# Optimization experiments

Hardware: AMD Instinct MI355X
Metric: run time of the kernel (lower is better)

## Reference

```python
import jax, jax.numpy as jnp
import numpy as np

B, N, D, H = 4, 2048, 256, 8
DH = D // H  # 32
EPS = 1e-5


def layernorm(x, g, b):
    mu = jnp.mean(x, axis=-1, keepdims=True)
    var = jnp.mean(jnp.square(x - mu), axis=-1, keepdims=True)
    return (x - mu) * jax.lax.rsqrt(var + EPS) * g + b


def setup_inputs() -> dict:
    key = jax.random.key(0)
    ks = jax.random.split(key, 16)
    s = 1.0 / np.sqrt(D)
    p = lambda k: jax.random.uniform(k, (D, D), jnp.float32, -s, s)
    return {
        "qdt": jax.random.normal(ks[0], (B, N, D), jnp.float32),
        "boxes": jax.random.normal(ks[1], (B, N, D), jnp.float32),
        "mask": jax.random.randint(ks[2], (N, N), 0, 2, jnp.int32),
        "Wq": p(ks[3]), "bq": jnp.zeros((D,), jnp.float32),
        "Wk": p(ks[4]), "bk": jnp.zeros((D,), jnp.float32),
        "Wv": p(ks[5]), "bv": jnp.zeros((D,), jnp.float32),
        "Wo": p(ks[6]), "bo": jnp.zeros((D,), jnp.float32),
        "W1": p(ks[7]), "b1": jnp.zeros((D,), jnp.float32),
        "W2": p(ks[8]), "b2": jnp.zeros((D,), jnp.float32),
        "g1": jnp.ones((D,), jnp.float32), "be1": jnp.zeros((D,), jnp.float32),
        "g2": jnp.ones((D,), jnp.float32), "be2": jnp.zeros((D,), jnp.float32),
    }


def reference(qdt, boxes, mask, Wq, bq, Wk, bk, Wv, bv, Wo, bo,
              W1, b1, W2, b2, g1, be1, g2, be2):
    # q = k = tgt = boxes + qdt  (dropout in eval mode -> identity)
    x = boxes + qdt  # [B,N,D]
    q = (x @ Wq + bq).reshape(B, N, H, DH)
    k = (x @ Wk + bk).reshape(B, N, H, DH)
    v = (x @ Wv + bv).reshape(B, N, H, DH)
    scores = jnp.einsum('bqhd,bkhd->bhqk', q, k) / np.sqrt(DH)
    # masked_fill(mask==0, -inf) then sigmoid  ==  sigmoid gated to 0 where masked
    attn = jnp.where(mask.astype(bool)[None, None, :, :],
                     jax.nn.sigmoid(scores), 0.0)
    o = jnp.einsum('bhqk,bkhd->bqhd', attn, v).reshape(B, N, D)
    attn_out = o @ Wo + bo
    tgt = layernorm(x + attn_out, g1, be1)
    ff = jax.nn.relu(tgt @ W1 + b1) @ W2 + b2
    tgt = layernorm(tgt + ff, g2, be2)
    return tgt
```

## Files before the change

### kernel.cpp

```cpp
#include <hip/hip_runtime.h>
#include <hip/hip_bf16.h>

typedef unsigned short u16;
typedef unsigned int u32;
typedef __attribute__((ext_vector_type(8))) short bf16x8;
typedef __attribute__((ext_vector_type(4))) float f32x4;

#define BB 4
#define NN 2048
#define DD 256
#define HH 8
#define LAMBDA (-0.2550351f)

__device__ inline u16 bfu(float f) {
  __hip_bfloat16 h = __float2bfloat16(f);
  return *reinterpret_cast<u16*>(&h);
}
__device__ inline bf16x8 asfrag(uint4 v) { return __builtin_bit_cast(bf16x8, v); }

__global__ __launch_bounds__(256) void prep_kernel(
    const float* __restrict__ qdt, const float* __restrict__ boxes,
    const int* __restrict__ mask,
    const float* __restrict__ Wq, const float* __restrict__ Wk, const float* __restrict__ Wv,
    const float* __restrict__ Wo, const float* __restrict__ W1, const float* __restrict__ W2,
    const float* __restrict__ bq, const float* __restrict__ bk, const float* __restrict__ bv,
    float* __restrict__ xp, u16* __restrict__ xb, unsigned char* __restrict__ m8,
    u16* __restrict__ wqkvT, u16* __restrict__ woT, u16* __restrict__ w1T, u16* __restrict__ w2T,
    float* __restrict__ bqkv) {
  const int bid = blockIdx.x, t = threadIdx.x;
  if (bid < 2048) {
    int i = bid * 256 + t;
    int row = i >> 6, q = i & 63;
    float4 a = ((const float4*)qdt)[i];
    float4 b = ((const float4*)boxes)[i];
    float4 v = make_float4(a.x + b.x, a.y + b.y, a.z + b.z, a.w + b.w);
    ((ushort4*)xb)[i] = make_ushort4(bfu(v.x), bfu(v.y), bfu(v.z), bfu(v.w));
    float* xr = xp + (size_t)row * 256;
    xr[((4*q+0) & 15) * 16 + ((4*q+0) >> 4)] = v.x;
    xr[((4*q+1) & 15) * 16 + ((4*q+1) >> 4)] = v.y;
    xr[((4*q+2) & 15) * 16 + ((4*q+2) >> 4)] = v.z;
    xr[((4*q+3) & 15) * 16 + ((4*q+3) >> 4)] = v.w;
  } else if (bid < 6144) {
    int i = (bid - 2048) * 256 + t;
    int4 m = ((const int4*)mask)[i];
    ((uchar4*)m8)[i] = make_uchar4((unsigned char)m.x, (unsigned char)m.y,
                                   (unsigned char)m.z, (unsigned char)m.w);
  } else {
    int i = (bid - 6144) * 256 + t;
    if (i < 196608) {
      int n = i >> 8, k = i & 255;
      const float* src = (n < 256) ? Wq : (n < 512 ? Wk : Wv);
      wqkvT[i] = bfu(src[k * 256 + (n & 255)]);
    } else if (i < 262144) {
      int j = i - 196608; int n = j >> 8, k = j & 255;
      woT[j] = bfu(Wo[k * 256 + n]);
    } else if (i < 327680) {
      int j = i - 262144; int n = j >> 8, k = j & 255;
      w1T[j] = bfu(W1[k * 256 + n]);
    } else if (i < 393216) {
      int j = i - 327680; int n = j >> 8, k = j & 255;
      w2T[j] = bfu(W2[k * 256 + n]);
    } else if (i < 393984) {
      int n = i - 393216;
      bqkv[n] = (n < 256) ? bq[n] : (n < 512 ? bk[n - 256] : bv[n - 512]);
    }
  }
}

__global__ __launch_bounds__(256) void gemm_qkvt_kernel(
    const u16* __restrict__ xb, const u16* __restrict__ wqkvT,
    const float* __restrict__ bqkv,
    u16* __restrict__ qout, u16* __restrict__ kout, u16* __restrict__ vtout) {
  __shared__ u16 At[64][264];
  __shared__ u16 Bs[64][264];
  const int bid = blockIdx.x;
  const bool isqk = bid < 1024;
  const u16* A  = isqk ? xb : (wqkvT + 512 * 256);
  const u16* Bt = isqk ? wqkvT : xb;
  const int m0 = isqk ? (bid >> 3) * 64 : ((bid - 1024) >> 7) * 64;
  const int n0 = isqk ? (bid & 7) * 64 : ((bid - 1024) & 127) * 64;
  const int t = threadIdx.x;
  {
    const int row = t >> 2, cb = (t & 3) * 64;
    const u16* ga = A  + (size_t)(m0 + row) * 256 + cb;
    const u16* gb = Bt + (size_t)(n0 + row) * 256 + cb;
#pragma unroll
    for (int i = 0; i < 8; ++i) {
      *(int4*)&At[row][cb + i * 8] = *(const int4*)(ga + i * 8);
      *(int4*)&Bs[row][cb + i * 8] = *(const int4*)(gb + i * 8);
    }
  }
  __syncthreads();
  const int w = t >> 6, l = t & 63, g = l >> 4, c = l & 15;
  f32x4 acc[4] = {};
#pragma unroll
  for (int kk = 0; kk < 256; kk += 32) {
    bf16x8 af = *(const bf16x8*)&At[w * 16 + c][kk + g * 8];
#pragma unroll
    for (int j = 0; j < 4; ++j) {
      bf16x8 bfr = *(const bf16x8*)&Bs[j * 16 + c][kk + g * 8];
      acc[j] = __builtin_amdgcn_mfma_f32_16x16x32_bf16(af, bfr, acc[j], 0, 0, 0);
    }
  }
  if (isqk) {
    if (n0 < 256) {
#pragma unroll
      for (int j = 0; j < 4; ++j)
#pragma unroll
        for (int r = 0; r < 4; ++r) {
          int m = m0 + w * 16 + g * 4 + r, n = n0 + j * 16 + c;
          qout[(size_t)m * 256 + n] = bfu((acc[j][r] + bqkv[n]) * LAMBDA);
        }
    } else {
#pragma unroll
      for (int j = 0; j < 4; ++j)
#pragma unroll
        for (int r = 0; r < 4; ++r) {
          int m = m0 + w * 16 + g * 4 + r, n = n0 + j * 16 + c;
          int ch = n - 256;
          kout[(size_t)((m >> 11) * 8 + (ch >> 5)) * 65536 + (size_t)(m & 2047) * 32 + (ch & 31)]
              = bfu(acc[j][r] + bqkv[n]);
        }
    }
  } else {
#pragma unroll
    for (int j = 0; j < 4; ++j)
#pragma unroll
      for (int r = 0; r < 4; ++r) {
        int m = m0 + w * 16 + g * 4 + r;
        int n = n0 + j * 16 + c;
        vtout[(size_t)m * 8192 + n] = bfu(acc[j][r] + bqkv[512 + m]);
      }
  }
}

__global__ __launch_bounds__(256) void attn_kernel(
    const u16* __restrict__ qb,
    const u16* __restrict__ kb,
    const u16* __restrict__ vtb,
    const unsigned char* __restrict__ m8,
    u16* __restrict__ ob) {
  __shared__ u32 Klds[2][64][20];
  __shared__ u32 Vlds[2][32][36];
  __shared__ unsigned char Mlds[2][128][64];
  __shared__ u32 Plds[4][32][36];

  const int bid = blockIdx.x;
  const int qt = bid & 15, h = (bid >> 4) & 7, b = bid >> 7;
  const int q0 = qt * 128;
  const int t = threadIdx.x, w = t >> 6, l = t & 63, g = l >> 4, c = l & 15;

  const bf16x8 qf0 = asfrag(*(const uint4*)(qb + (size_t)(b * NN + q0 + 32 * w + c) * 256 + h * 32 + 8 * g));
  const bf16x8 qf1 = asfrag(*(const uint4*)(qb + (size_t)(b * NN + q0 + 32 * w + 16 + c) * 256 + h * 32 + 8 * g));
  f32x4 oacc[2][2] = {};

  const int srowK = t >> 2, ssegK = t & 3;
  const int srowV = t >> 3, ssegV = t & 7;
  const int msrow = t >> 1, mhalf = t & 1;
  const u16* kg = kb + (size_t)(b * 8 + h) * 65536 + srowK * 32 + ssegK * 8;
  const u16* vg = vtb + (size_t)(h * 32 + srowV) * 8192 + (size_t)b * NN + ssegV * 8;
  const unsigned char* mg = m8 + (size_t)(q0 + msrow) * NN + mhalf * 32;

  const int rotM = 8 * (msrow & 7);
  const int mbA0 = (32 * mhalf + rotM) & 63, mbA1 = (mbA0 + 8) & 63;
  const int mbB0 = (mbA0 + 16) & 63,         mbB1 = (mbA0 + 24) & 63;

  uint4 krg = *(const uint4*)kg;
  uint4 vrg = *(const uint4*)vg;
  uint4 mrgA = *(const uint4*)mg;
  uint4 mrgB = *(const uint4*)(mg + 16);
  *(uint4*)&Klds[0][srowK][ssegK * 4] = krg;
  *(uint4*)&Vlds[0][srowV][ssegV * 4] = vrg;
  *(uint2*)&Mlds[0][msrow][mbA0] = make_uint2(mrgA.x, mrgA.y);
  *(uint2*)&Mlds[0][msrow][mbA1] = make_uint2(mrgA.z, mrgA.w);
  *(uint2*)&Mlds[0][msrow][mbB0] = make_uint2(mrgB.x, mrgB.y);
  *(uint2*)&Mlds[0][msrow][mbB1] = make_uint2(mrgB.z, mrgB.w);
  __syncthreads();

  const f32x4 zf = {0.f, 0.f, 0.f, 0.f};
  u32* Pw = &Plds[w][0][0];

  for (int it = 0; it < 32; ++it) {
    const int cur = it & 1;
    if (it < 31) {
      const int kt = (it + 1) * 64;
      krg = *(const uint4*)(kg + (size_t)kt * 32);
      vrg = *(const uint4*)(vg + kt);
      mrgA = *(const uint4*)(mg + kt);
      mrgB = *(const uint4*)(mg + kt + 16);
    }
#pragma unroll
    for (int tt = 0; tt < 4; ++tt) {
      bf16x8 kf = asfrag(*(const uint4*)&Klds[cur][16 * tt + c][4 * g]);
      f32x4 s0 = __builtin_amdgcn_mfma_f32_16x16x32_bf16(kf, qf0, zf, 0, 0, 0);
      f32x4 s1 = __builtin_amdgcn_mfma_f32_16x16x32_bf16(kf, qf1, zf, 0, 0, 0);
      const int mpos = (16 * tt + 4 * g + 8 * (c & 7)) & 63;
      u32 mdw0 = *(const u32*)&Mlds[cur][32 * w + c][mpos];
      u32 mdw1 = *(const u32*)&Mlds[cur][32 * w + 16 + c][mpos];
      {
        float p0 = (float)(mdw0 & 0xffu) * __builtin_amdgcn_rcpf(1.f + __builtin_amdgcn_exp2f(s0[0]));
        float p1 = (float)((mdw0 >> 8) & 0xffu) * __builtin_amdgcn_rcpf(1.f + __builtin_amdgcn_exp2f(s0[1]));
        float p2 = (float)((mdw0 >> 16) & 0xffu) * __builtin_amdgcn_rcpf(1.f + __builtin_amdgcn_exp2f(s0[2]));
        float p3 = (float)(mdw0 >> 24) * __builtin_amdgcn_rcpf(1.f + __builtin_amdgcn_exp2f(s0[3]));
        u32 w0, w1;
        asm("v_cvt_pk_bf16_f32 %0, %1, %2" : "=v"(w0) : "v"(p0), "v"(p1));
        asm("v_cvt_pk_bf16_f32 %0, %1, %2" : "=v"(w1) : "v"(p2), "v"(p3));
        *(uint2*)&Pw[c * 36 + 8 * tt + 2 * g] = make_uint2(w0, w1);
      }
      {
        float p0 = (float)(mdw1 & 0xffu) * __builtin_amdgcn_rcpf(1.f + __builtin_amdgcn_exp2f(s1[0]));
        float p1 = (float)((mdw1 >> 8) & 0xffu) * __builtin_amdgcn_rcpf(1.f + __builtin_amdgcn_exp2f(s1[1]));
        float p2 = (float)((mdw1 >> 16) & 0xffu) * __builtin_amdgcn_rcpf(1.f + __builtin_amdgcn_exp2f(s1[2]));
        float p3 = (float)(mdw1 >> 24) * __builtin_amdgcn_rcpf(1.f + __builtin_amdgcn_exp2f(s1[3]));
        u32 w0, w1;
        asm("v_cvt_pk_bf16_f32 %0, %1, %2" : "=v"(w0) : "v"(p0), "v"(p1));
        asm("v_cvt_pk_bf16_f32 %0, %1, %2" : "=v"(w1) : "v"(p2), "v"(p3));
        *(uint2*)&Pw[(16 + c) * 36 + 8 * tt + 2 * g] = make_uint2(w0, w1);
      }
    }
    asm volatile("s_waitcnt lgkmcnt(0)" ::: "memory");
    __builtin_amdgcn_sched_barrier(0);
#pragma unroll
    for (int kk = 0; kk < 2; ++kk) {
      bf16x8 pf0 = asfrag(*(const uint4*)&Pw[c * 36 + 16 * kk + 4 * g]);
      bf16x8 pf1 = asfrag(*(const uint4*)&Pw[(16 + c) * 36 + 16 * kk + 4 * g]);
#pragma unroll
      for (int d0 = 0; d0 < 2; ++d0) {
        bf16x8 vf = asfrag(*(const uint4*)&Vlds[cur][16 * d0 + c][16 * kk + 4 * g]);
        oacc[0][d0] = __builtin_amdgcn_mfma_f32_16x16x32_bf16(pf0, vf, oacc[0][d0], 0, 0, 0);
        oacc[1][d0] = __builtin_amdgcn_mfma_f32_16x16x32_bf16(pf1, vf, oacc[1][d0], 0, 0, 0);
      }
    }
    if (it < 31) {
      *(uint4*)&Klds[cur ^ 1][srowK][ssegK * 4] = krg;
      *(uint4*)&Vlds[cur ^ 1][srowV][ssegV * 4] = vrg;
      *(uint2*)&Mlds[cur ^ 1][msrow][mbA0] = make_uint2(mrgA.x, mrgA.y);
      *(uint2*)&Mlds[cur ^ 1][msrow][mbA1] = make_uint2(mrgA.z, mrgA.w);
      *(uint2*)&Mlds[cur ^ 1][msrow][mbB0] = make_uint2(mrgB.x, mrgB.y);
      *(uint2*)&Mlds[cur ^ 1][msrow][mbB1] = make_uint2(mrgB.z, mrgB.w);
    }
    __syncthreads();
  }

#pragma unroll
  for (int f = 0; f < 2; ++f) {
    const size_t obase = (size_t)(b * NN + q0 + 32 * w + 16 * f) * 256 + h * 32;
#pragma unroll
    for (int d0 = 0; d0 < 2; ++d0)
#pragma unroll
      for (int r = 0; r < 4; ++r)
        ob[obase + (size_t)(4 * g + r) * 256 + 16 * d0 + c] = bfu(oacc[f][d0][r]);
  }
}

__global__ __launch_bounds__(256) void tail_kernel(
    const u16* __restrict__ obuf, const u16* __restrict__ woT,
    const u16* __restrict__ w1T, const u16* __restrict__ w2T,
    const float* __restrict__ xp,
    const float* __restrict__ bo, const float* __restrict__ b1, const float* __restrict__ b2,
    const float* __restrict__ g1, const float* __restrict__ be1,
    const float* __restrict__ g2, const float* __restrict__ be2,
    float* __restrict__ out) {
  __shared__ u16 A[32][264];
  __shared__ float PS1[32][4], PS2[32][4];
  const int t = threadIdx.x, w = t >> 6, l = t & 63, g = l >> 4, c = l & 15;
  const int m0 = blockIdx.x * 32;
  const int n0 = w * 64;
  const f32x4 zf4 = {0.f, 0.f, 0.f, 0.f};

  {
    const int srow = t >> 3, sseg = t & 7;
#pragma unroll
    for (int i = 0; i < 4; ++i) {
      uint4 v = *(const uint4*)(obuf + (size_t)(m0 + srow) * 256 + (sseg + 8 * i) * 8);
      *(uint4*)&A[srow][(sseg + 8 * i) * 8] = v;
    }
  }
  __syncthreads();

  f32x4 acc[2][4], t1[2][4];
  float mean[2][4], inv[2][4];

#pragma unroll
  for (int rg = 0; rg < 2; ++rg)
#pragma unroll
    for (int j = 0; j < 4; ++j) acc[rg][j] = zf4;
#pragma unroll
  for (int kk = 0; kk < 256; kk += 32) {
    bf16x8 af0 = *(const bf16x8*)&A[c][kk + 8 * g];
    bf16x8 af1 = *(const bf16x8*)&A[16 + c][kk + 8 * g];
#pragma unroll
    for (int j = 0; j < 4; ++j) {
      bf16x8 bfr = asfrag(*(const uint4*)(woT + (size_t)(n0 + 16 * j + c) * 256 + kk + 8 * g));
      acc[0][j] = __builtin_amdgcn_mfma_f32_16x16x32_bf16(af0, bfr, acc[0][j], 0, 0, 0);
      acc[1][j] = __builtin_amdgcn_mfma_f32_16x16x32_bf16(af1, bfr, acc[1][j], 0, 0, 0);
    }
  }
  {
    float bov[4];
#pragma unroll
    for (int j = 0; j < 4; ++j) bov[j] = bo[n0 + 16 * j + c];
#pragma unroll
    for (int rg = 0; rg < 2; ++rg)
#pragma unroll
      for (int r = 0; r < 4; ++r) {
        const int rl = 16 * rg + 4 * g + r;
        float4 xq = ((const float4*)(xp + (size_t)(m0 + rl) * 256 + c * 16))[w];
        float xa[4] = {xq.x, xq.y, xq.z, xq.w};
        float a1 = 0.f, a2 = 0.f;
#pragma unroll
        for (int j = 0; j < 4; ++j) {
          float z = acc[rg][j][r] + bov[j] + xa[j];
          t1[rg][j][r] = z;
          a1 += z; a2 += z * z;
        }
#pragma unroll
        for (int off = 1; off < 16; off <<= 1) {
          a1 += __shfl_xor(a1, off);
          a2 += __shfl_xor(a2, off);
        }
        if (c == 0) { PS1[rl][w] = a1; PS2[rl][w] = a2; }
      }
  }
  __syncthreads();
#pragma unroll
  for (int rg = 0; rg < 2; ++rg)
#pragma unroll
    for (int r = 0; r < 4; ++r) {
      const int rl = 16 * rg + 4 * g + r;
      float s1 = PS1[rl][0] + PS1[rl][1] + PS1[rl][2] + PS1[rl][3];
      float s2 = PS2[rl][0] + PS2[rl][1] + PS2[rl][2] + PS2[rl][3];
      mean[rg][r] = s1 * (1.f / 256.f);
      inv[rg][r] = rsqrtf(s2 * (1.f / 256.f) - mean[rg][r] * mean[rg][r] + 1e-5f);
    }
#pragma unroll
  for (int j = 0; j < 4; ++j) {
    const int n = n0 + 16 * j + c;
    const float gv = g1[n], bev = be1[n];
#pragma unroll
    for (int rg = 0; rg < 2; ++rg)
#pragma unroll
      for (int r = 0; r < 4; ++r) {
        float v = (t1[rg][j][r] - mean[rg][r]) * inv[rg][r] * gv + bev;
        t1[rg][j][r] = v;
        A[16 * rg + 4 * g + r][n] = bfu(v);
      }
  }
  __syncthreads();

#pragma unroll
  for (int rg = 0; rg < 2; ++rg)
#pragma unroll
    for (int j = 0; j < 4; ++j) acc[rg][j] = zf4;
#pragma unroll
  for (int kk = 0; kk < 256; kk += 32) {
    bf16x8 af0 = *(const bf16x8*)&A[c][kk + 8 * g];
    bf16x8 af1 = *(const bf16x8*)&A[16 + c][kk + 8 * g];
#pragma unroll
    for (int j = 0; j < 4; ++j) {
      bf16x8 bfr = asfrag(*(const uint4*)(w1T + (size_t)(n0 + 16 * j + c) * 256 + kk + 8 * g));
      acc[0][j] = __builtin_amdgcn_mfma_f32_16x16x32_bf16(af0, bfr, acc[0][j], 0, 0, 0);
      acc[1][j] = __builtin_amdgcn_mfma_f32_16x16x32_bf16(af1, bfr, acc[1][j], 0, 0, 0);
    }
  }
  __syncthreads();
#pragma unroll
  for (int j = 0; j < 4; ++j) {
    const int n = n0 + 16 * j + c;
    const float bv = b1[n];
#pragma unroll
    for (int rg = 0; rg < 2; ++rg)
#pragma unroll
      for (int r = 0; r < 4; ++r) {
        float v = acc[rg][j][r] + bv;
        A[16 * rg + 4 * g + r][n] = bfu(v > 0.f ? v : 0.f);
      }
  }
  __syncthreads();

#pragma unroll
  for (int rg = 0; rg < 2; ++rg)
#pragma unroll
    for (int j = 0; j < 4; ++j) acc[rg][j] = zf4;
#pragma unroll
  for (int kk = 0; kk < 256; kk += 32) {
    bf16x8 af0 = *(const bf16x8*)&A[c][kk + 8 * g];
    bf16x8 af1 = *(const bf16x8*)&A[16 + c][kk + 8 * g];
#pragma unroll
    for (int j = 0; j < 4; ++j) {
      bf16x8 bfr = asfrag(*(const uint4*)(w2T + (size_t)(n0 + 16 * j + c) * 256 + kk + 8 * g));
      acc[0][j] = __builtin_amdgcn_mfma_f32_16x16x32_bf16(af0, bfr, acc[0][j], 0, 0, 0);
      acc[1][j] = __builtin_amdgcn_mfma_f32_16x16x32_bf16(af1, bfr, acc[1][j], 0, 0, 0);
    }
  }
  {
    float b2v[4];
#pragma unroll
    for (int j = 0; j < 4; ++j) b2v[j] = b2[n0 + 16 * j + c];
#pragma unroll
    for (int rg = 0; rg < 2; ++rg)
#pragma unroll
      for (int r = 0; r < 4; ++r) {
        const int rl = 16 * rg + 4 * g + r;
        float a1 = 0.f, a2 = 0.f;
#pragma unroll
        for (int j = 0; j < 4; ++j) {
          float z = acc[rg][j][r] + b2v[j] + t1[rg][j][r];
          t1[rg][j][r] = z;
          a1 += z; a2 += z * z;
        }
#pragma unroll
        for (int off = 1; off < 16; off <<= 1) {
          a1 += __shfl_xor(a1, off);
          a2 += __shfl_xor(a2, off);
        }
        if (c == 0) { PS1[rl][w] = a1; PS2[rl][w] = a2; }
      }
  }
  __syncthreads();
#pragma unroll
  for (int rg = 0; rg < 2; ++rg)
#pragma unroll
    for (int r = 0; r < 4; ++r) {
      const int rl = 16 * rg + 4 * g + r;
      float s1 = PS1[rl][0] + PS1[rl][1] + PS1[rl][2] + PS1[rl][3];
      float s2 = PS2[rl][0] + PS2[rl][1] + PS2[rl][2] + PS2[rl][3];
      mean[rg][r] = s1 * (1.f / 256.f);
      inv[rg][r] = rsqrtf(s2 * (1.f / 256.f) - mean[rg][r] * mean[rg][r] + 1e-5f);
    }
#pragma unroll
  for (int j = 0; j < 4; ++j) {
    const int n = n0 + 16 * j + c;
    const float gv = g2[n], bev = be2[n];
#pragma unroll
    for (int rg = 0; rg < 2; ++rg)
#pragma unroll
      for (int r = 0; r < 4; ++r)
        out[(size_t)(m0 + 16 * rg + 4 * g + r) * 256 + n]
            = (t1[rg][j][r] - mean[rg][r]) * inv[rg][r] * gv + bev;
  }
}

extern "C" void kernel_launch(void* const* d_in, const int* in_sizes, int n_in,
                              void* d_out, int out_size, void* d_ws, size_t ws_size,
                              hipStream_t stream) {
  const float* qdt   = (const float*)d_in[0];
  const float* boxes = (const float*)d_in[1];
  const int*   mask  = (const int*)d_in[2];
  const float* Wq = (const float*)d_in[3];
  const float* bq = (const float*)d_in[4];
  const float* Wk = (const float*)d_in[5];
  const float* bk = (const float*)d_in[6];
  const float* Wv = (const float*)d_in[7];
  const float* bv = (const float*)d_in[8];
  const float* Wo = (const float*)d_in[9];
  const float* bo = (const float*)d_in[10];
  const float* W1 = (const float*)d_in[11];
  const float* b1 = (const float*)d_in[12];
  const float* W2 = (const float*)d_in[13];
  const float* b2 = (const float*)d_in[14];
  const float* g1  = (const float*)d_in[15];
  const float* be1 = (const float*)d_in[16];
  const float* g2  = (const float*)d_in[17];
  const float* be2 = (const float*)d_in[18];

  char* ws = (char*)d_ws;
  float* xp    = (float*)(ws + 0);
  u16*   xb    = (u16*)  (ws + 8388608);
  u16*   qbuf  = (u16*)  (ws + 12582912);
  u16*   kbuf  = (u16*)  (ws + 16777216);
  u16*   vtbuf = (u16*)  (ws + 20971520);
  u16*   obuf  = (u16*)  (ws + 25165824);
  u16*   wqkvT = (u16*)  (ws + 46137344);
  u16*   woT   = (u16*)  (ws + 46530560);
  u16*   w1T   = (u16*)  (ws + 46661632);
  u16*   w2T   = (u16*)  (ws + 46792704);
  float* bqkv  = (float*)(ws + 46923776);
  unsigned char* m8 = (unsigned char*)(ws + 46926848);

  prep_kernel<<<7683, 256, 0, stream>>>(qdt, boxes, mask, Wq, Wk, Wv, Wo, W1, W2,
                                        bq, bk, bv, xp, xb, m8,
                                        wqkvT, woT, w1T, w2T, bqkv);
  gemm_qkvt_kernel<<<1536, 256, 0, stream>>>(xb, wqkvT, bqkv, qbuf, kbuf, vtbuf);
  attn_kernel<<<512, 256, 0, stream>>>(qbuf, kbuf, vtbuf, m8, obuf);
  tail_kernel<<<256, 256, 0, stream>>>(obuf, woT, w1T, w2T, xp,
                                       bo, b1, b2, g1, be1, g2, be2, (float*)d_out);
}
```

Before: 115.5 us.

## Pack attention mask into bitmask and read it directly into registers

The prep kernel now packs the int32 mask into one bit per element (32 per word) instead of one byte per element. The attention kernel loads each query row's 64 mask bits per key tile straight into registers and drops the shared-memory mask staging and its LDS reads and writes. This cuts mask traffic to global memory and LDS, and frees LDS space that could allow higher occupancy. In exchange, prep threads do strided 128-byte reads per thread, and the attention inner loop adds shift-and-mask work to extract each bit.

```diff
diff --git a/kernel.cpp b/kernel.cpp
--- a/kernel.cpp
+++ b/kernel.cpp
@@ -24,7 +24,7 @@
     const float* __restrict__ Wq, const float* __restrict__ Wk, const float* __restrict__ Wv,
     const float* __restrict__ Wo, const float* __restrict__ W1, const float* __restrict__ W2,
     const float* __restrict__ bq, const float* __restrict__ bk, const float* __restrict__ bv,
-    float* __restrict__ xp, u16* __restrict__ xb, unsigned char* __restrict__ m8,
+    float* __restrict__ xp, u16* __restrict__ xb, u32* __restrict__ m1,
     u16* __restrict__ wqkvT, u16* __restrict__ woT, u16* __restrict__ w1T, u16* __restrict__ w2T,
     float* __restrict__ bqkv) {
   const int bid = blockIdx.x, t = threadIdx.x;
@@ -40,13 +40,21 @@
     xr[((4*q+1) & 15) * 16 + ((4*q+1) >> 4)] = v.y;
     xr[((4*q+2) & 15) * 16 + ((4*q+2) >> 4)] = v.z;
     xr[((4*q+3) & 15) * 16 + ((4*q+3) >> 4)] = v.w;
-  } else if (bid < 6144) {
+  } else if (bid < 2560) {
     int i = (bid - 2048) * 256 + t;
-    int4 m = ((const int4*)mask)[i];
-    ((uchar4*)m8)[i] = make_uchar4((unsigned char)m.x, (unsigned char)m.y,
-                                   (unsigned char)m.z, (unsigned char)m.w);
+    const int* src = mask + (size_t)i * 32;
+    u32 bits = 0;
+#pragma unroll
+    for (int q4 = 0; q4 < 8; ++q4) {
+      int4 m = *(const int4*)(src + q4 * 4);
+      bits |= (m.x ? 1u : 0u) << (4 * q4);
+      bits |= (m.y ? 1u : 0u) << (4 * q4 + 1);
+      bits |= (m.z ? 1u : 0u) << (4 * q4 + 2);
+      bits |= (m.w ? 1u : 0u) << (4 * q4 + 3);
+    }
+    m1[i] = bits;
   } else {
-    int i = (bid - 6144) * 256 + t;
+    int i = (bid - 2560) * 256 + t;
     if (i < 196608) {
       int n = i >> 8, k = i & 255;
       const float* src = (n < 256) ? Wq : (n < 512 ? Wk : Wv);
@@ -138,11 +146,10 @@
     const u16* __restrict__ qb,
     const u16* __restrict__ kb,
     const u16* __restrict__ vtb,
-    const unsigned char* __restrict__ m8,
+    const u32* __restrict__ m1,
     u16* __restrict__ ob) {
   __shared__ u32 Klds[2][64][20];
   __shared__ u32 Vlds[2][32][36];
-  __shared__ unsigned char Mlds[2][128][64];
   __shared__ u32 Plds[4][32][36];
 
   const int bid = blockIdx.x;
@@ -156,25 +163,17 @@
 
   const int srowK = t >> 2, ssegK = t & 3;
   const int srowV = t >> 3, ssegV = t & 7;
-  const int msrow = t >> 1, mhalf = t & 1;
   const u16* kg = kb + (size_t)(b * 8 + h) * 65536 + srowK * 32 + ssegK * 8;
   const u16* vg = vtb + (size_t)(h * 32 + srowV) * 8192 + (size_t)b * NN + ssegV * 8;
-  const unsigned char* mg = m8 + (size_t)(q0 + msrow) * NN + mhalf * 32;
-
-  const int rotM = 8 * (msrow & 7);
-  const int mbA0 = (32 * mhalf + rotM) & 63, mbA1 = (mbA0 + 8) & 63;
-  const int mbB0 = (mbA0 + 16) & 63,         mbB1 = (mbA0 + 24) & 63;
+  const u32* mr0 = m1 + (size_t)(q0 + 32 * w + c) * 64;
+  const u32* mr1 = m1 + (size_t)(q0 + 32 * w + 16 + c) * 64;
 
   uint4 krg = *(const uint4*)kg;
   uint4 vrg = *(const uint4*)vg;
-  uint4 mrgA = *(const uint4*)mg;
-  uint4 mrgB = *(const uint4*)(mg + 16);
+  uint2 mc0 = *(const uint2*)mr0;
+  uint2 mc1 = *(const uint2*)mr1;
   *(uint4*)&Klds[0][srowK][ssegK * 4] = krg;
   *(uint4*)&Vlds[0][srowV][ssegV * 4] = vrg;
-  *(uint2*)&Mlds[0][msrow][mbA0] = make_uint2(mrgA.x, mrgA.y);
-  *(uint2*)&Mlds[0][msrow][mbA1] = make_uint2(mrgA.z, mrgA.w);
-  *(uint2*)&Mlds[0][msrow][mbB0] = make_uint2(mrgB.x, mrgB.y);
-  *(uint2*)&Mlds[0][msrow][mbB1] = make_uint2(mrgB.z, mrgB.w);
   __syncthreads();
 
   const f32x4 zf = {0.f, 0.f, 0.f, 0.f};
@@ -182,36 +181,37 @@
 
   for (int it = 0; it < 32; ++it) {
     const int cur = it & 1;
+    uint2 mn0, mn1;
     if (it < 31) {
       const int kt = (it + 1) * 64;
       krg = *(const uint4*)(kg + (size_t)kt * 32);
       vrg = *(const uint4*)(vg + kt);
-      mrgA = *(const uint4*)(mg + kt);
-      mrgB = *(const uint4*)(mg + kt + 16);
+      mn0 = *(const uint2*)(mr0 + (it + 1) * 2);
+      mn1 = *(const uint2*)(mr1 + (it + 1) * 2);
     }
 #pragma unroll
     for (int tt = 0; tt < 4; ++tt) {
       bf16x8 kf = asfrag(*(const uint4*)&Klds[cur][16 * tt + c][4 * g]);
       f32x4 s0 = __builtin_amdgcn_mfma_f32_16x16x32_bf16(kf, qf0, zf, 0, 0, 0);
       f32x4 s1 = __builtin_amdgcn_mfma_f32_16x16x32_bf16(kf, qf1, zf, 0, 0, 0);
-      const int mpos = (16 * tt + 4 * g + 8 * (c & 7)) & 63;
-      u32 mdw0 = *(const u32*)&Mlds[cur][32 * w + c][mpos];
-      u32 mdw1 = *(const u32*)&Mlds[cur][32 * w + 16 + c][mpos];
+      const u32 wd0 = (tt < 2) ? mc0.x : mc0.y;
+      const u32 wd1 = (tt < 2) ? mc1.x : mc1.y;
+      const int off = 16 * (tt & 1) + 4 * g;
       {
-        float p0 = (float)(mdw0 & 0xffu) * __builtin_amdgcn_rcpf(1.f + __builtin_amdgcn_exp2f(s0[0]));
-        float p1 = (float)((mdw0 >> 8) & 0xffu) * __builtin_amdgcn_rcpf(1.f + __builtin_amdgcn_exp2f(s0[1]));
-        float p2 = (float)((mdw0 >> 16) & 0xffu) * __builtin_amdgcn_rcpf(1.f + __builtin_amdgcn_exp2f(s0[2]));
-        float p3 = (float)(mdw0 >> 24) * __builtin_amdgcn_rcpf(1.f + __builtin_amdgcn_exp2f(s0[3]));
+        float p0 = (float)((wd0 >> (off + 0)) & 1u) * __builtin_amdgcn_rcpf(1.f + __builtin_amdgcn_exp2f(s0[0]));
+        float p1 = (float)((wd0 >> (off + 1)) & 1u) * __builtin_amdgcn_rcpf(1.f + __builtin_amdgcn_exp2f(s0[1]));
+        float p2 = (float)((wd0 >> (off + 2)) & 1u) * __builtin_amdgcn_rcpf(1.f + __builtin_amdgcn_exp2f(s0[2]));
+        float p3 = (float)((wd0 >> (off + 3)) & 1u) * __builtin_amdgcn_rcpf(1.f + __builtin_amdgcn_exp2f(s0[3]));
         u32 w0, w1;
         asm("v_cvt_pk_bf16_f32 %0, %1, %2" : "=v"(w0) : "v"(p0), "v"(p1));
         asm("v_cvt_pk_bf16_f32 %0, %1, %2" : "=v"(w1) : "v"(p2), "v"(p3));
         *(uint2*)&Pw[c * 36 + 8 * tt + 2 * g] = make_uint2(w0, w1);
       }
       {
-        float p0 = (float)(mdw1 & 0xffu) * __builtin_amdgcn_rcpf(1.f + __builtin_amdgcn_exp2f(s1[0]));
-        float p1 = (float)((mdw1 >> 8) & 0xffu) * __builtin_amdgcn_rcpf(1.f + __builtin_amdgcn_exp2f(s1[1]));
-        float p2 = (float)((mdw1 >> 16) & 0xffu) * __builtin_amdgcn_rcpf(1.f + __builtin_amdgcn_exp2f(s1[2]));
-        float p3 = (float)(mdw1 >> 24) * __builtin_amdgcn_rcpf(1.f + __builtin_amdgcn_exp2f(s1[3]));
+        float p0 = (float)((wd1 >> (off + 0)) & 1u) * __builtin_amdgcn_rcpf(1.f + __builtin_amdgcn_exp2f(s1[0]));
+        float p1 = (float)((wd1 >> (off + 1)) & 1u) * __builtin_amdgcn_rcpf(1.f + __builtin_amdgcn_exp2f(s1[1]));
+        float p2 = (float)((wd1 >> (off + 2)) & 1u) * __builtin_amdgcn_rcpf(1.f + __builtin_amdgcn_exp2f(s1[2]));
+        float p3 = (float)((wd1 >> (off + 3)) & 1u) * __builtin_amdgcn_rcpf(1.f + __builtin_amdgcn_exp2f(s1[3]));
         u32 w0, w1;
         asm("v_cvt_pk_bf16_f32 %0, %1, %2" : "=v"(w0) : "v"(p0), "v"(p1));
         asm("v_cvt_pk_bf16_f32 %0, %1, %2" : "=v"(w1) : "v"(p2), "v"(p3));
@@ -234,10 +234,7 @@
     if (it < 31) {
       *(uint4*)&Klds[cur ^ 1][srowK][ssegK * 4] = krg;
       *(uint4*)&Vlds[cur ^ 1][srowV][ssegV * 4] = vrg;
-      *(uint2*)&Mlds[cur ^ 1][msrow][mbA0] = make_uint2(mrgA.x, mrgA.y);
-      *(uint2*)&Mlds[cur ^ 1][msrow][mbA1] = make_uint2(mrgA.z, mrgA.w);
-      *(uint2*)&Mlds[cur ^ 1][msrow][mbB0] = make_uint2(mrgB.x, mrgB.y);
-      *(uint2*)&Mlds[cur ^ 1][msrow][mbB1] = make_uint2(mrgB.z, mrgB.w);
+      mc0 = mn0; mc1 = mn1;
     }
     __syncthreads();
   }
@@ -476,13 +473,13 @@
   u16*   w1T   = (u16*)  (ws + 46661632);
   u16*   w2T   = (u16*)  (ws + 46792704);
   float* bqkv  = (float*)(ws + 46923776);
-  unsigned char* m8 = (unsigned char*)(ws + 46926848);
-
-  prep_kernel<<<7683, 256, 0, stream>>>(qdt, boxes, mask, Wq, Wk, Wv, Wo, W1, W2,
-                                        bq, bk, bv, xp, xb, m8,
+  u32*   m1    = (u32*)  (ws + 46926848);
+
+  prep_kernel<<<4099, 256, 0, stream>>>(qdt, boxes, mask, Wq, Wk, Wv, Wo, W1, W2,
+                                        bq, bk, bv, xp, xb, m1,
                                         wqkvT, woT, w1T, w2T, bqkv);
   gemm_qkvt_kernel<<<1536, 256, 0, stream>>>(xb, wqkvT, bqkv, qbuf, kbuf, vtbuf);
-  attn_kernel<<<512, 256, 0, stream>>>(qbuf, kbuf, vtbuf, m8, obuf);
+  attn_kernel<<<512, 256, 0, stream>>>(qbuf, kbuf, vtbuf, m1, obuf);
   tail_kernel<<<256, 256, 0, stream>>>(obuf, woT, w1T, w2T, xp,
                                        bo, b1, b2, g1, be1, g2, be2, (float*)d_out);
 }
```

Result: no change. 115.4 us (-0.1%).
